# Performance work log

Hardware: AMD Instinct MI355X
Metric: run time of the kernel (lower is better)

Reference implementation:

```python
import jax, jax.numpy as jnp
import numpy as np

NUM_HEADS = 8
NUM_POINTS = 4


def setup_inputs() -> dict:
    key = jax.random.key(0)
    ks = jax.random.split(key, 10)
    B, H, W, D = 8, 64, 64, 256
    N = H * W
    nh, P = NUM_HEADS, NUM_POINTS

    def xavier(k, shape):
        fan_in, fan_out = shape[0], shape[1]
        lim = float(np.sqrt(6.0 / (fan_in + fan_out)))
        return jax.random.uniform(k, shape, jnp.float32, -lim, lim)

    x = jax.random.normal(ks[0], (B, N, D), jnp.float32)
    qkv_w = xavier(ks[1], (D, 3 * D))
    qkv_b = jnp.zeros((3 * D,), jnp.float32)
    # offset network is zero-init in the module; use small random weights so the
    # deformable sampling is actually exercised (offsets nonzero).
    off_w = jax.random.normal(ks[2], (D, nh * P * 2), jnp.float32) * 0.01
    off_b = jnp.zeros((nh * P * 2,), jnp.float32)
    attw_w = xavier(ks[3], (D, nh * P))
    attw_b = jnp.zeros((nh * P,), jnp.float32)
    proj_w = xavier(ks[4], (D, D))
    proj_b = jnp.zeros((D,), jnp.float32)
    return {
        "x": x, "qkv_w": qkv_w, "qkv_b": qkv_b,
        "off_w": off_w, "off_b": off_b,
        "attw_w": attw_w, "attw_b": attw_b,
        "proj_w": proj_w, "proj_b": proj_b,
        "H": 64, "W": 64,
    }


def _deformable_forward(x, qkv_w, qkv_b, off_w, off_b, attw_w, attw_b, proj_w, proj_b, H, W):
    B, N, D = x.shape
    nh, P = NUM_HEADS, NUM_POINTS
    hd = D // nh

    qkv = x @ qkv_w + qkv_b                      # [B,N,3D] (q,k computed but unused, as in the original)
    v = qkv[..., 2 * D:].reshape(B, N, nh, hd)   # [B,N,nh,hd]

    offsets = jnp.tanh((x @ off_w + off_b).reshape(B, N, nh, P, 2)) * 2.0

    ys, xs = jnp.meshgrid(jnp.arange(H, dtype=x.dtype), jnp.arange(W, dtype=x.dtype), indexing="ij")
    ref = jnp.stack([xs, ys], axis=-1).reshape(N, 2)          # [N,2] (x,y) pixel coords
    loc = ref[None, :, None, None, :] + offsets               # [B,N,nh,P,2] pixel coords
    # (module normalizes to [-1,1] then grid_sample align_corners=True un-normalizes
    #  back to exactly these pixel coordinates, so we sample at `loc` directly)

    # value as flat spatial map per head: [B,nh,hd,N], n = y*W + x
    vf = v.transpose(0, 2, 3, 1).reshape(B, nh, hd, N)

    gx, gy = loc[..., 0], loc[..., 1]
    x0 = jnp.floor(gx); y0 = jnp.floor(gy)
    x1 = x0 + 1.0;      y1 = y0 + 1.0
    wx1 = gx - x0; wx0 = 1.0 - wx1
    wy1 = gy - y0; wy0 = 1.0 - wy1

    def corner(xi, yi, w):
        # bilinear corner with zeros padding: zero weight if corner out of bounds
        valid = (xi >= 0) & (xi < W) & (yi >= 0) & (yi < H)
        idx = (jnp.clip(yi, 0, H - 1) * W + jnp.clip(xi, 0, W - 1)).astype(jnp.int32)
        idx2 = idx.transpose(0, 2, 1, 3).reshape(B, nh, N * P)          # [B,nh,N*P]
        g = jnp.take_along_axis(vf, idx2[:, :, None, :], axis=3)        # [B,nh,hd,N*P]
        w2 = (w * valid.astype(x.dtype)).transpose(0, 2, 1, 3).reshape(B, nh, 1, N * P)
        return g * w2

    sampled = (corner(x0, y0, wx0 * wy0) + corner(x1, y0, wx1 * wy0)
               + corner(x0, y1, wx0 * wy1) + corner(x1, y1, wx1 * wy1))
    sampled = sampled.reshape(B, nh, hd, N, P)

    attn = jax.nn.softmax((x @ attw_w + attw_b).reshape(B, N, nh, P), axis=-1)
    out = jnp.einsum("bhcnp,bnhp->bnhc", sampled, attn).reshape(B, N, D)
    return out @ proj_w + proj_b


def reference(x, qkv_w, qkv_b, off_w, off_b, attw_w, attw_b, proj_w, proj_b, H, W):
    return _deformable_forward(x, qkv_w, qkv_b, off_w, off_b, attw_w, attw_b, proj_w, proj_b, H, W)
```

## Files before the change

### kernel.cpp

```cpp
#include <hip/hip_runtime.h>
#include <hip/hip_bf16.h>
#include <cmath>

#define NN 4096
typedef __attribute__((ext_vector_type(8))) short short8;
typedef __attribute__((ext_vector_type(4))) float f32x4;

__device__ __forceinline__ float bf2f(unsigned short u) {
  union { unsigned int i; float f; } c; c.i = ((unsigned int)u) << 16; return c.f;
}

__global__ __launch_bounds__(256) void cvt_w(
    const float* __restrict__ qkv_w, const float* __restrict__ off_w,
    const float* __restrict__ attw_w, const float* __restrict__ proj_w,
    __hip_bfloat16* __restrict__ wcatT, __hip_bfloat16* __restrict__ pjT)
{
  const int t = threadIdx.x;
  if (blockIdx.x < 256) {
    int k = blockIdx.x;
    wcatT[t * 256 + k] = __float2bfloat16(qkv_w[k * 768 + 512 + t]);
    if (t < 128) {
      int c2 = 256 + t;
      float v = 0.f;
      if (c2 < 320)      v = off_w[k * 64 + (c2 - 256)];
      else if (c2 < 352) v = attw_w[k * 32 + (c2 - 320)];
      wcatT[c2 * 256 + k] = __float2bfloat16(v);
    }
  } else {
    int k = blockIdx.x - 256;
    pjT[t * 256 + k] = __float2bfloat16(proj_w[k * 256 + t]);
  }
}

__global__ __launch_bounds__(256) void gemm_voff(
    const float* __restrict__ x,
    const __hip_bfloat16* __restrict__ wcatT,
    const float* __restrict__ vbias,
    const float* __restrict__ off_b, const float* __restrict__ attw_b,
    __hip_bfloat16* __restrict__ vb,
    unsigned int* __restrict__ table)
{
  __shared__ float smemf[8960];
  short* As = (short*)smemf;
  short* Bs = As + 64 * 40;
  float (*L)[100] = (float(*)[100])smemf;

  const int t = threadIdx.x;
  const int m0 = blockIdx.x * 64;
  const int wave = t >> 6, lane = t & 63, q = lane >> 4, ln = lane & 15;
  const int wn = wave * 96;

  f32x4 acc[4][6] = {};

  const int arow = t >> 2, aseg = t & 3;
  const float* apg = x + (size_t)(m0 + arow) * 256 + aseg * 8;

  for (int k0 = 0; k0 < 256; k0 += 32) {
    float4 f0 = *(const float4*)(apg + k0);
    float4 f1 = *(const float4*)(apg + k0 + 4);
    alignas(16) __hip_bfloat16 cv[8] = {
      __float2bfloat16(f0.x), __float2bfloat16(f0.y), __float2bfloat16(f0.z), __float2bfloat16(f0.w),
      __float2bfloat16(f1.x), __float2bfloat16(f1.y), __float2bfloat16(f1.z), __float2bfloat16(f1.w)};
    *(int4*)&As[arow * 40 + aseg * 8] = *(int4*)cv;
#pragma unroll
    for (int i = 0; i < 6; ++i) {
      int u = t + i * 256;
      int brow = u >> 2, bseg = u & 3;
      *(int4*)&Bs[brow * 40 + bseg * 8] =
          *(const int4*)&wcatT[(size_t)brow * 256 + k0 + bseg * 8];
    }
    __syncthreads();
    short8 a[4], b[6];
#pragma unroll
    for (int i = 0; i < 4; ++i) a[i] = *(const short8*)&As[(i * 16 + ln) * 40 + q * 8];
#pragma unroll
    for (int j = 0; j < 6; ++j) b[j] = *(const short8*)&Bs[(wn + j * 16 + ln) * 40 + q * 8];
#pragma unroll
    for (int i = 0; i < 4; ++i)
#pragma unroll
      for (int j = 0; j < 6; ++j)
        acc[i][j] = __builtin_amdgcn_mfma_f32_16x16x32_bf16(a[i], b[j], acc[i][j], 0, 0, 0);
    __syncthreads();
  }

#pragma unroll
  for (int j = 0; j < 6; ++j) {
    int col = wn + j * 16 + ln;
    if (col < 256) {
      float bv = vbias[col];
#pragma unroll
      for (int i = 0; i < 4; ++i) {
        int rowb = m0 + i * 16 + q * 4;
#pragma unroll
        for (int r = 0; r < 4; ++r)
          vb[(size_t)(rowb + r) * 256 + col] = __float2bfloat16(acc[i][j][r] + bv);
      }
    } else if (col < 352) {
      int lc = col - 256;
      float bv = (lc < 64) ? off_b[lc] : attw_b[lc - 64];
#pragma unroll
      for (int i = 0; i < 4; ++i)
#pragma unroll
        for (int r = 0; r < 4; ++r)
          L[i * 16 + q * 4 + r][lc] = acc[i][j][r] + bv;
    }
  }
  __syncthreads();

#pragma unroll
  for (int it = 0; it < 2; ++it) {
    int pl = t + it * 256;
    int rr = pl >> 3, h = pl & 7;
    int row = m0 + rr;
    int nl = row & (NN - 1);
    float refx = (float)(nl & 63);
    float refy = (float)(nl >> 6);

    float a0 = L[rr][64 + h * 4 + 0], a1 = L[rr][64 + h * 4 + 1];
    float a2 = L[rr][64 + h * 4 + 2], a3 = L[rr][64 + h * 4 + 3];
    float mx = fmaxf(fmaxf(a0, a1), fmaxf(a2, a3));
    float e0 = expf(a0 - mx), e1 = expf(a1 - mx), e2 = expf(a2 - mx), e3 = expf(a3 - mx);
    float inv = 1.f / (e0 + e1 + e2 + e3);
    float at[4] = {e0 * inv, e1 * inv, e2 * inv, e3 * inv};

    alignas(16) unsigned short idxs[16];
    alignas(16) _Float16 wsv[16];
#pragma unroll
    for (int p = 0; p < 4; ++p) {
      float gx = refx + 2.f * tanhf(L[rr][h * 8 + p * 2 + 0]);
      float gy = refy + 2.f * tanhf(L[rr][h * 8 + p * 2 + 1]);
      float x0f = floorf(gx), y0f = floorf(gy);
      int x0 = (int)x0f, y0 = (int)y0f;
      int x1 = x0 + 1,   y1 = y0 + 1;
      float wx1 = gx - x0f, wx0 = 1.f - wx1;
      float wy1 = gy - y0f, wy0 = 1.f - wy1;
      int cx0 = min(max(x0, 0), 63), cx1 = min(max(x1, 0), 63);
      int cy0 = min(max(y0, 0), 63), cy1 = min(max(y1, 0), 63);
      float vx0 = (x0 >= 0 && x0 <= 63) ? 1.f : 0.f;
      float vx1 = (x1 >= 0 && x1 <= 63) ? 1.f : 0.f;
      float vy0 = (y0 >= 0 && y0 <= 63) ? 1.f : 0.f;
      float vy1 = (y1 >= 0 && y1 <= 63) ? 1.f : 0.f;
      float ap = at[p];
      idxs[p * 4 + 0] = (unsigned short)(cy0 * 64 + cx0);
      idxs[p * 4 + 1] = (unsigned short)(cy0 * 64 + cx1);
      idxs[p * 4 + 2] = (unsigned short)(cy1 * 64 + cx0);
      idxs[p * 4 + 3] = (unsigned short)(cy1 * 64 + cx1);
      wsv[p * 4 + 0] = (_Float16)(ap * wx0 * wy0 * vx0 * vy0);
      wsv[p * 4 + 1] = (_Float16)(ap * wx1 * wy0 * vx1 * vy0);
      wsv[p * 4 + 2] = (_Float16)(ap * wx0 * wy1 * vx0 * vy1);
      wsv[p * 4 + 3] = (_Float16)(ap * wx1 * wy1 * vx1 * vy1);
    }
    uint4* dst = (uint4*)(table + ((size_t)row * 8 + h) * 16);
    dst[0] = *(uint4*)&idxs[0];
    dst[1] = *(uint4*)&idxs[8];
    dst[2] = *(uint4*)&wsv[0];
    dst[3] = *(uint4*)&wsv[8];
  }
}

__global__ __launch_bounds__(256) void gemm_sproj(
    const __hip_bfloat16* __restrict__ vb,
    const unsigned int* __restrict__ table,
    const __hip_bfloat16* __restrict__ pjT,
    const float* __restrict__ bias,
    float* __restrict__ out)
{
  __shared__ short ytile[64 * 264];
  __shared__ short Bs[256 * 40];
  const int t = threadIdx.x;
  const int m0 = blockIdx.x * 64;
  const int wave = t >> 6, lane = t & 63, q = lane >> 4, ln = lane & 15;
  const int wn = wave * 64;
  const int b = m0 >> 12;

#pragma unroll
  for (int i = 0; i < 8; ++i) {
    int tau = t + i * 256;
    int r = tau >> 5, h = (tau >> 2) & 7, g = tau & 3;
    int row = m0 + r;
    const uint4* tp = (const uint4*)(table + ((size_t)row * 8 + h) * 16);
    uint4 e0 = tp[0], e1 = tp[1];
    uint4 e2 = tp[2], e3 = tp[3];
    const unsigned int iw[8] = {e0.x, e0.y, e0.z, e0.w, e1.x, e1.y, e1.z, e1.w};
    const unsigned int ww[8] = {e2.x, e2.y, e2.z, e2.w, e3.x, e3.y, e3.z, e3.w};
    const char* vbase = (const char*)(vb + ((size_t)b * NN * 256) + h * 32 + g * 8);
    float accg[8] = {};
#pragma unroll
    for (int j = 0; j < 16; ++j) {
      unsigned int idx = (iw[j >> 1] >> ((j & 1) * 16)) & 0xffffu;
      union { unsigned int u; _Float16 h2[2]; } wu; wu.u = ww[j >> 1];
      float w = (float)wu.h2[j & 1];
      int4 pk = *(const int4*)(vbase + (size_t)idx * 512);
      const unsigned short* uu = (const unsigned short*)&pk;
#pragma unroll
      for (int c = 0; c < 8; ++c) accg[c] += w * bf2f(uu[c]);
    }
    alignas(16) __hip_bfloat16 o[8];
#pragma unroll
    for (int c = 0; c < 8; ++c) o[c] = __float2bfloat16(accg[c]);
    *(int4*)&ytile[r * 264 + h * 32 + g * 8] = *(int4*)o;
  }
  __syncthreads();

  f32x4 acc[4][4] = {};
  for (int k0 = 0; k0 < 256; k0 += 32) {
#pragma unroll
    for (int i = 0; i < 4; ++i) {
      int u = t + i * 256;
      int brow = u >> 2, bseg = u & 3;
      *(int4*)&Bs[brow * 40 + bseg * 8] =
          *(const int4*)&pjT[(size_t)brow * 256 + k0 + bseg * 8];
    }
    __syncthreads();
    short8 a[4], bfr[4];
#pragma unroll
    for (int i = 0; i < 4; ++i) a[i] = *(const short8*)&ytile[(i * 16 + ln) * 264 + k0 + q * 8];
#pragma unroll
    for (int j = 0; j < 4; ++j) bfr[j] = *(const short8*)&Bs[(wn + j * 16 + ln) * 40 + q * 8];
#pragma unroll
    for (int i = 0; i < 4; ++i)
#pragma unroll
      for (int j = 0; j < 4; ++j)
        acc[i][j] = __builtin_amdgcn_mfma_f32_16x16x32_bf16(a[i], bfr[j], acc[i][j], 0, 0, 0);
    __syncthreads();
  }

#pragma unroll
  for (int j = 0; j < 4; ++j) {
    int col = wn + j * 16 + ln;
    float bv = bias[col];
#pragma unroll
    for (int i = 0; i < 4; ++i) {
      int rowb = m0 + i * 16 + q * 4;
#pragma unroll
      for (int r = 0; r < 4; ++r)
        out[(size_t)(rowb + r) * 256 + col] = acc[i][j][r] + bv;
    }
  }
}

extern "C" void kernel_launch(void* const* d_in, const int* in_sizes, int n_in,
                              void* d_out, int out_size, void* d_ws, size_t ws_size,
                              hipStream_t stream) {
  const float* x      = (const float*)d_in[0];
  const float* qkv_w  = (const float*)d_in[1];
  const float* qkv_b  = (const float*)d_in[2];
  const float* off_w  = (const float*)d_in[3];
  const float* off_b  = (const float*)d_in[4];
  const float* attw_w = (const float*)d_in[5];
  const float* attw_b = (const float*)d_in[6];
  const float* proj_w = (const float*)d_in[7];
  const float* proj_b = (const float*)d_in[8];
  float* out = (float*)d_out;

  char* ws = (char*)d_ws;
  __hip_bfloat16* vb    = (__hip_bfloat16*)(ws);
  unsigned int*   table = (unsigned int*)  (ws + 16777216);
  __hip_bfloat16* wcatT = (__hip_bfloat16*)(ws + 33554432);
  __hip_bfloat16* pjT   = (__hip_bfloat16*)(ws + 33751040);

  cvt_w<<<512, 256, 0, stream>>>(qkv_w, off_w, attw_w, proj_w, wcatT, pjT);
  gemm_voff<<<512, 256, 0, stream>>>(x, wcatT, qkv_b + 512, off_b, attw_b, vb, table);
  gemm_sproj<<<512, 256, 0, stream>>>(vb, table, pjT, proj_b, out);
}
```

Baseline: 169.8 us.

## Halve GEMM row tiles to 32 and register-prefetch next K slab

Both fused GEMM kernels now process 32 rows per block instead of 64, doubling the grid to 1024 blocks so the 256 CUs get more blocks and more waves in flight. The K loops now load the next 32-wide K slab into registers while the current slab is consumed, overlapping global loads with MFMA work. In exchange, each block re-reads the full weight matrix for half as many rows, doubling weight traffic from L2. The removed sync after the gather phase relies on the first in-loop barrier instead.

```diff
diff --git a/kernel.cpp b/kernel.cpp
--- a/kernel.cpp
+++ b/kernel.cpp
@@ -40,43 +40,52 @@
     __hip_bfloat16* __restrict__ vb,
     unsigned int* __restrict__ table)
 {
-  __shared__ float smemf[8960];
+  __shared__ float smemf[8320];
   short* As = (short*)smemf;
-  short* Bs = As + 64 * 40;
+  short* Bs = As + 32 * 40;
   float (*L)[100] = (float(*)[100])smemf;
 
   const int t = threadIdx.x;
-  const int m0 = blockIdx.x * 64;
+  const int m0 = blockIdx.x * 32;
   const int wave = t >> 6, lane = t & 63, q = lane >> 4, ln = lane & 15;
   const int wn = wave * 96;
 
-  f32x4 acc[4][6] = {};
-
-  const int arow = t >> 2, aseg = t & 3;
-  const float* apg = x + (size_t)(m0 + arow) * 256 + aseg * 8;
+  f32x4 acc[2][6] = {};
+
+  const int arow = t >> 3, akseg = t & 7;
+  const float* apg = x + (size_t)(m0 + arow) * 256 + akseg * 4;
+  int brow[6], bseg[6];
+#pragma unroll
+  for (int i = 0; i < 6; ++i) { int u = t + i * 256; brow[i] = u >> 2; bseg[i] = u & 3; }
+
+  float4 a_pf = *(const float4*)(apg);
+  int4 b_pf[6];
+#pragma unroll
+  for (int i = 0; i < 6; ++i)
+    b_pf[i] = *(const int4*)&wcatT[(size_t)brow[i] * 256 + bseg[i] * 8];
 
   for (int k0 = 0; k0 < 256; k0 += 32) {
-    float4 f0 = *(const float4*)(apg + k0);
-    float4 f1 = *(const float4*)(apg + k0 + 4);
-    alignas(16) __hip_bfloat16 cv[8] = {
-      __float2bfloat16(f0.x), __float2bfloat16(f0.y), __float2bfloat16(f0.z), __float2bfloat16(f0.w),
-      __float2bfloat16(f1.x), __float2bfloat16(f1.y), __float2bfloat16(f1.z), __float2bfloat16(f1.w)};
-    *(int4*)&As[arow * 40 + aseg * 8] = *(int4*)cv;
-#pragma unroll
-    for (int i = 0; i < 6; ++i) {
-      int u = t + i * 256;
-      int brow = u >> 2, bseg = u & 3;
-      *(int4*)&Bs[brow * 40 + bseg * 8] =
-          *(const int4*)&wcatT[(size_t)brow * 256 + k0 + bseg * 8];
-    }
-    __syncthreads();
-    short8 a[4], b[6];
-#pragma unroll
-    for (int i = 0; i < 4; ++i) a[i] = *(const short8*)&As[(i * 16 + ln) * 40 + q * 8];
+    alignas(8) __hip_bfloat16 cv[4] = {
+      __float2bfloat16(a_pf.x), __float2bfloat16(a_pf.y),
+      __float2bfloat16(a_pf.z), __float2bfloat16(a_pf.w)};
+    *(int2*)&As[arow * 40 + akseg * 4] = *(int2*)cv;
+#pragma unroll
+    for (int i = 0; i < 6; ++i)
+      *(int4*)&Bs[brow[i] * 40 + bseg[i] * 8] = b_pf[i];
+    __syncthreads();
+    if (k0 < 224) {
+      a_pf = *(const float4*)(apg + k0 + 32);
+#pragma unroll
+      for (int i = 0; i < 6; ++i)
+        b_pf[i] = *(const int4*)&wcatT[(size_t)brow[i] * 256 + k0 + 32 + bseg[i] * 8];
+    }
+    short8 a[2], b[6];
+#pragma unroll
+    for (int i = 0; i < 2; ++i) a[i] = *(const short8*)&As[(i * 16 + ln) * 40 + q * 8];
 #pragma unroll
     for (int j = 0; j < 6; ++j) b[j] = *(const short8*)&Bs[(wn + j * 16 + ln) * 40 + q * 8];
 #pragma unroll
-    for (int i = 0; i < 4; ++i)
+    for (int i = 0; i < 2; ++i)
 #pragma unroll
       for (int j = 0; j < 6; ++j)
         acc[i][j] = __builtin_amdgcn_mfma_f32_16x16x32_bf16(a[i], b[j], acc[i][j], 0, 0, 0);
@@ -89,7 +98,7 @@
     if (col < 256) {
       float bv = vbias[col];
 #pragma unroll
-      for (int i = 0; i < 4; ++i) {
+      for (int i = 0; i < 2; ++i) {
         int rowb = m0 + i * 16 + q * 4;
 #pragma unroll
         for (int r = 0; r < 4; ++r)
@@ -99,7 +108,7 @@
       int lc = col - 256;
       float bv = (lc < 64) ? off_b[lc] : attw_b[lc - 64];
 #pragma unroll
-      for (int i = 0; i < 4; ++i)
+      for (int i = 0; i < 2; ++i)
 #pragma unroll
         for (int r = 0; r < 4; ++r)
           L[i * 16 + q * 4 + r][lc] = acc[i][j][r] + bv;
@@ -107,10 +116,8 @@
   }
   __syncthreads();
 
-#pragma unroll
-  for (int it = 0; it < 2; ++it) {
-    int pl = t + it * 256;
-    int rr = pl >> 3, h = pl & 7;
+  {
+    int rr = t >> 3, h = t & 7;
     int row = m0 + rr;
     int nl = row & (NN - 1);
     float refx = (float)(nl & 63);
@@ -165,16 +172,16 @@
     const float* __restrict__ bias,
     float* __restrict__ out)
 {
-  __shared__ short ytile[64 * 264];
+  __shared__ short ytile[32 * 264];
   __shared__ short Bs[256 * 40];
   const int t = threadIdx.x;
-  const int m0 = blockIdx.x * 64;
+  const int m0 = blockIdx.x * 32;
   const int wave = t >> 6, lane = t & 63, q = lane >> 4, ln = lane & 15;
   const int wn = wave * 64;
   const int b = m0 >> 12;
 
 #pragma unroll
-  for (int i = 0; i < 8; ++i) {
+  for (int i = 0; i < 4; ++i) {
     int tau = t + i * 256;
     int r = tau >> 5, h = (tau >> 2) & 7, g = tau & 3;
     int row = m0 + r;
@@ -200,25 +207,33 @@
     for (int c = 0; c < 8; ++c) o[c] = __float2bfloat16(accg[c]);
     *(int4*)&ytile[r * 264 + h * 32 + g * 8] = *(int4*)o;
   }
-  __syncthreads();
-
-  f32x4 acc[4][4] = {};
+
+  int brow[4], bseg[4];
+#pragma unroll
+  for (int i = 0; i < 4; ++i) { int u = t + i * 256; brow[i] = u >> 2; bseg[i] = u & 3; }
+  int4 b_pf[4];
+#pragma unroll
+  for (int i = 0; i < 4; ++i)
+    b_pf[i] = *(const int4*)&pjT[(size_t)brow[i] * 256 + bseg[i] * 8];
+
+  f32x4 acc[2][4] = {};
   for (int k0 = 0; k0 < 256; k0 += 32) {
 #pragma unroll
-    for (int i = 0; i < 4; ++i) {
-      int u = t + i * 256;
-      int brow = u >> 2, bseg = u & 3;
-      *(int4*)&Bs[brow * 40 + bseg * 8] =
-          *(const int4*)&pjT[(size_t)brow * 256 + k0 + bseg * 8];
-    }
-    __syncthreads();
-    short8 a[4], bfr[4];
-#pragma unroll
-    for (int i = 0; i < 4; ++i) a[i] = *(const short8*)&ytile[(i * 16 + ln) * 264 + k0 + q * 8];
+    for (int i = 0; i < 4; ++i)
+      *(int4*)&Bs[brow[i] * 40 + bseg[i] * 8] = b_pf[i];
+    __syncthreads();
+    if (k0 < 224) {
+#pragma unroll
+      for (int i = 0; i < 4; ++i)
+        b_pf[i] = *(const int4*)&pjT[(size_t)brow[i] * 256 + k0 + 32 + bseg[i] * 8];
+    }
+    short8 a[2], bfr[4];
+#pragma unroll
+    for (int i = 0; i < 2; ++i) a[i] = *(const short8*)&ytile[(i * 16 + ln) * 264 + k0 + q * 8];
 #pragma unroll
     for (int j = 0; j < 4; ++j) bfr[j] = *(const short8*)&Bs[(wn + j * 16 + ln) * 40 + q * 8];
 #pragma unroll
-    for (int i = 0; i < 4; ++i)
+    for (int i = 0; i < 2; ++i)
 #pragma unroll
       for (int j = 0; j < 4; ++j)
         acc[i][j] = __builtin_amdgcn_mfma_f32_16x16x32_bf16(a[i], bfr[j], acc[i][j], 0, 0, 0);
@@ -230,7 +245,7 @@
     int col = wn + j * 16 + ln;
     float bv = bias[col];
 #pragma unroll
-    for (int i = 0; i < 4; ++i) {
+    for (int i = 0; i < 2; ++i) {
       int rowb = m0 + i * 16 + q * 4;
 #pragma unroll
       for (int r = 0; r < 4; ++r)
@@ -260,6 +275,6 @@
   __hip_bfloat16* pjT   = (__hip_bfloat16*)(ws + 33751040);
 
   cvt_w<<<512, 256, 0, stream>>>(qkv_w, off_w, attw_w, proj_w, wcatT, pjT);
-  gemm_voff<<<512, 256, 0, stream>>>(x, wcatT, qkv_b + 512, off_b, attw_b, vb, table);
-  gemm_sproj<<<512, 256, 0, stream>>>(vb, table, pjT, proj_b, out);
-}
+  gemm_voff<<<1024, 256, 0, stream>>>(x, wcatT, qkv_b + 512, off_b, attw_b, vb, table);
+  gemm_sproj<<<1024, 256, 0, stream>>>(vb, table, pjT, proj_b, out);
+}
```

Result: slower. 221.6 us (+30.5%).

## Tile weight transpose via LDS and enlarge gemm_voff tile to 128 rows

Applied to the files above, without the earlier changes.

The weight conversion kernel now transposes 64x64 tiles through shared memory with coalesced float4 reads and 16-byte writes, replacing strided scalar stores, and runs on 40 blocks instead of 512. The fused V/offset GEMM moves to 512-thread blocks covering 128 rows, with waves split 2x4 over M and N so each weight tile loaded into LDS is reused across twice as many rows. The cost is fewer blocks (256) and more LDS per block, which may lower occupancy. The A-load indexing (arow = t>>2) now covers 128 rows with 512 threads, which is consistent.

```diff
diff --git a/kernel.cpp b/kernel.cpp
--- a/kernel.cpp
+++ b/kernel.cpp
@@ -15,24 +15,47 @@
     const float* __restrict__ attw_w, const float* __restrict__ proj_w,
     __hip_bfloat16* __restrict__ wcatT, __hip_bfloat16* __restrict__ pjT)
 {
+  __shared__ short T[64][72];
   const int t = threadIdx.x;
-  if (blockIdx.x < 256) {
-    int k = blockIdx.x;
-    wcatT[t * 256 + k] = __float2bfloat16(qkv_w[k * 768 + 512 + t]);
-    if (t < 128) {
-      int c2 = 256 + t;
-      float v = 0.f;
-      if (c2 < 320)      v = off_w[k * 64 + (c2 - 256)];
-      else if (c2 < 352) v = attw_w[k * 32 + (c2 - 320)];
-      wcatT[c2 * 256 + k] = __float2bfloat16(v);
-    }
-  } else {
-    int k = blockIdx.x - 256;
-    pjT[t * 256 + k] = __float2bfloat16(proj_w[k * 256 + t]);
-  }
-}
-
-__global__ __launch_bounds__(256) void gemm_voff(
+  const int tile = blockIdx.x;
+  const bool isP = tile >= 24;
+  const int ct = isP ? (tile - 24) & 3 : tile % 6;
+  const int kt = isP ? (tile - 24) >> 2 : tile / 6;
+  const int c0 = ct * 64, k0 = kt * 64;
+
+#pragma unroll
+  for (int r = 0; r < 4; ++r) {
+    int kk = r * 16 + (t >> 4);
+    int cc = (t & 15) * 4;
+    int k = k0 + kk, gc = c0 + cc;
+    float4 v;
+    if (isP) {
+      v = *(const float4*)&proj_w[(size_t)k * 256 + gc];
+    } else if (gc < 256) {
+      v = *(const float4*)&qkv_w[(size_t)k * 768 + 512 + gc];
+    } else if (gc < 320) {
+      v = *(const float4*)&off_w[(size_t)k * 64 + (gc - 256)];
+    } else if (gc < 352) {
+      v = *(const float4*)&attw_w[(size_t)k * 32 + (gc - 320)];
+    } else {
+      v = make_float4(0.f, 0.f, 0.f, 0.f);
+    }
+    T[cc + 0][kk] = ((__hip_bfloat16_raw)__float2bfloat16(v.x)).x;
+    T[cc + 1][kk] = ((__hip_bfloat16_raw)__float2bfloat16(v.y)).x;
+    T[cc + 2][kk] = ((__hip_bfloat16_raw)__float2bfloat16(v.z)).x;
+    T[cc + 3][kk] = ((__hip_bfloat16_raw)__float2bfloat16(v.w)).x;
+  }
+  __syncthreads();
+
+  {
+    int c = t >> 2, kseg = t & 3;
+    __hip_bfloat16* dst = (isP ? pjT : wcatT) + (size_t)(c0 + c) * 256 + k0 + kseg * 16;
+    *(int4*)(dst)     = *(int4*)&T[c][kseg * 16];
+    *(int4*)(dst + 8) = *(int4*)&T[c][kseg * 16 + 8];
+  }
+}
+
+__global__ __launch_bounds__(512) void gemm_voff(
     const float* __restrict__ x,
     const __hip_bfloat16* __restrict__ wcatT,
     const float* __restrict__ vbias,
@@ -40,15 +63,15 @@
     __hip_bfloat16* __restrict__ vb,
     unsigned int* __restrict__ table)
 {
-  __shared__ float smemf[8960];
+  __shared__ float smemf[12800];
   short* As = (short*)smemf;
-  short* Bs = As + 64 * 40;
+  short* Bs = As + 128 * 40;
   float (*L)[100] = (float(*)[100])smemf;
 
   const int t = threadIdx.x;
-  const int m0 = blockIdx.x * 64;
+  const int m0 = blockIdx.x * 128;
   const int wave = t >> 6, lane = t & 63, q = lane >> 4, ln = lane & 15;
-  const int wn = wave * 96;
+  const int wm = (wave & 1) * 64, wn = (wave >> 1) * 96;
 
   f32x4 acc[4][6] = {};
 
@@ -63,8 +86,8 @@
       __float2bfloat16(f1.x), __float2bfloat16(f1.y), __float2bfloat16(f1.z), __float2bfloat16(f1.w)};
     *(int4*)&As[arow * 40 + aseg * 8] = *(int4*)cv;
 #pragma unroll
-    for (int i = 0; i < 6; ++i) {
-      int u = t + i * 256;
+    for (int i = 0; i < 3; ++i) {
+      int u = t + i * 512;
       int brow = u >> 2, bseg = u & 3;
       *(int4*)&Bs[brow * 40 + bseg * 8] =
           *(const int4*)&wcatT[(size_t)brow * 256 + k0 + bseg * 8];
@@ -72,7 +95,7 @@
     __syncthreads();
     short8 a[4], b[6];
 #pragma unroll
-    for (int i = 0; i < 4; ++i) a[i] = *(const short8*)&As[(i * 16 + ln) * 40 + q * 8];
+    for (int i = 0; i < 4; ++i) a[i] = *(const short8*)&As[(wm + i * 16 + ln) * 40 + q * 8];
 #pragma unroll
     for (int j = 0; j < 6; ++j) b[j] = *(const short8*)&Bs[(wn + j * 16 + ln) * 40 + q * 8];
 #pragma unroll
@@ -90,7 +113,7 @@
       float bv = vbias[col];
 #pragma unroll
       for (int i = 0; i < 4; ++i) {
-        int rowb = m0 + i * 16 + q * 4;
+        int rowb = m0 + wm + i * 16 + q * 4;
 #pragma unroll
         for (int r = 0; r < 4; ++r)
           vb[(size_t)(rowb + r) * 256 + col] = __float2bfloat16(acc[i][j][r] + bv);
@@ -102,14 +125,14 @@
       for (int i = 0; i < 4; ++i)
 #pragma unroll
         for (int r = 0; r < 4; ++r)
-          L[i * 16 + q * 4 + r][lc] = acc[i][j][r] + bv;
+          L[wm + i * 16 + q * 4 + r][lc] = acc[i][j][r] + bv;
     }
   }
   __syncthreads();
 
 #pragma unroll
   for (int it = 0; it < 2; ++it) {
-    int pl = t + it * 256;
+    int pl = t + it * 512;
     int rr = pl >> 3, h = pl & 7;
     int row = m0 + rr;
     int nl = row & (NN - 1);
@@ -259,7 +282,7 @@
   __hip_bfloat16* wcatT = (__hip_bfloat16*)(ws + 33554432);
   __hip_bfloat16* pjT   = (__hip_bfloat16*)(ws + 33751040);
 
-  cvt_w<<<512, 256, 0, stream>>>(qkv_w, off_w, attw_w, proj_w, wcatT, pjT);
-  gemm_voff<<<512, 256, 0, stream>>>(x, wcatT, qkv_b + 512, off_b, attw_b, vb, table);
+  cvt_w<<<40, 256, 0, stream>>>(qkv_w, off_w, attw_w, proj_w, wcatT, pjT);
+  gemm_voff<<<256, 512, 0, stream>>>(x, wcatT, qkv_b + 512, off_b, attw_b, vb, table);
   gemm_sproj<<<512, 256, 0, stream>>>(vb, table, pjT, proj_b, out);
 }
```

New measurement: 160.4 us. 1.06x faster.
